# Kernel tuning notes

Measured on AMD Instinct MI355X. Metric: run time of the kernel, lower is better.

## Reference

```python
import jax, jax.numpy as jnp
import numpy as np

D_MODEL, N_HEADS, D_FF = 1024, 16, 4096
B, S = 2, 2048
EPS = 1e-6


def setup_inputs() -> dict:
    key = jax.random.key(0)
    ks = jax.random.split(key, 8)
    sc = 0.02
    x = jax.random.normal(ks[0], (B, S, D_MODEL), dtype=jnp.float32)
    Wq = jax.random.normal(ks[1], (D_MODEL, D_MODEL), dtype=jnp.float32) * sc
    Wk = jax.random.normal(ks[2], (D_MODEL, D_MODEL), dtype=jnp.float32) * sc
    Wv = jax.random.normal(ks[3], (D_MODEL, D_MODEL), dtype=jnp.float32) * sc
    Wo = jax.random.normal(ks[4], (D_MODEL, D_MODEL), dtype=jnp.float32) * sc
    W1 = jax.random.normal(ks[5], (D_MODEL, D_FF), dtype=jnp.float32) * sc
    W2 = jax.random.normal(ks[6], (D_FF, D_MODEL), dtype=jnp.float32) * sc
    z = lambda n: jnp.zeros((n,), dtype=jnp.float32)
    return {
        'x': x,
        'Wq': Wq, 'bq': z(D_MODEL), 'Wk': Wk, 'bk': z(D_MODEL),
        'Wv': Wv, 'bv': z(D_MODEL), 'Wo': Wo, 'bo': z(D_MODEL),
        'W1': W1, 'b1': z(D_FF), 'W2': W2, 'b2': z(D_MODEL),
        'alpha1': jnp.ones((D_MODEL,), jnp.float32), 'beta1': z(D_MODEL),
        'alpha2': jnp.ones((D_MODEL,), jnp.float32), 'beta2': z(D_MODEL),
    }


def _layernorm(y, alpha, beta):
    # torch.std is Bessel-corrected (N-1); original divides by (std + eps)
    d = y.shape[-1]
    m = jnp.mean(y, axis=-1, keepdims=True)
    c = y - m
    std = jnp.sqrt(jnp.sum(c * c, axis=-1, keepdims=True) / (d - 1))
    return alpha * c / (std + EPS) + beta


def reference(x, Wq, bq, Wk, bk, Wv, bv, Wo, bo, W1, b1, W2, b2,
              alpha1, beta1, alpha2, beta2):
    Bx, Sx, D = x.shape
    H = N_HEADS
    dk = D // H
    # projections -> [B, H, S, dk]
    q = (x @ Wq + bq).reshape(Bx, Sx, H, dk).transpose(0, 2, 1, 3)
    k = (x @ Wk + bk).reshape(Bx, Sx, H, dk).transpose(0, 2, 1, 3)
    v = (x @ Wv + bv).reshape(Bx, Sx, H, dk).transpose(0, 2, 1, 3)
    scores = jnp.einsum('bhqd,bhkd->bhqk', q, k) / np.sqrt(dk).astype(np.float32)
    attn = jax.nn.softmax(scores, axis=-1)  # [B, H, S, S]
    ctx = jnp.einsum('bhqk,bhkd->bhqd', attn, v)
    ctx = ctx.transpose(0, 2, 1, 3).reshape(Bx, Sx, D)
    attn_out = _layernorm(x + (ctx @ Wo + bo), alpha1, beta1)
    ff = jax.nn.relu(attn_out @ W1 + b1) @ W2 + b2
    enc_out = _layernorm(attn_out + ff, alpha2, beta2)
    return enc_out, attn
```

## Files before the change

kernel.cpp:

```cpp
#include <hip/hip_runtime.h>

typedef _Float16 h8 __attribute__((ext_vector_type(8)));
typedef float f4 __attribute__((ext_vector_type(4)));
typedef unsigned short u16;
typedef unsigned short us8 __attribute__((ext_vector_type(8)));

#define MFMA16(a, b, c) __builtin_amdgcn_mfma_f32_16x16x32_f16(a, b, c, 0, 0, 0)

static __device__ __forceinline__ float bf2f(u16 u) {
  unsigned int x = ((unsigned int)u) << 16;
  return __builtin_bit_cast(float, x);
}
static __device__ __forceinline__ u16 f2bf(float f) {
  unsigned int x = __builtin_bit_cast(unsigned int, f);
  x += 0x7fffu + ((x >> 16) & 1u);
  return (u16)(x >> 16);
}

static __device__ __forceinline__ void gload16(const void* g, void* l) {
  __builtin_amdgcn_global_load_lds((const __attribute__((address_space(1))) void*)g,
                                   (__attribute__((address_space(3))) void*)l, 16, 0, 0);
}

__global__ void detect_dtype(const void* __restrict__ alpha1, int* __restrict__ flag) {
  u16 u = ((const u16*)alpha1)[0];
  *flag = (u == 0x3F80u) ? 1 : (u == 0x3C00u ? 2 : 0);
}

__global__ __launch_bounds__(256) void cvt_to_f16(const void* __restrict__ in,
                                                  _Float16* __restrict__ out, int n,
                                                  const int* __restrict__ flag) {
  int f = *flag;
  int i = (blockIdx.x * 256 + threadIdx.x) * 8;
  if (i >= n) return;
  h8 o;
  if (f == 1) {
    us8 v = *(const us8*)((const u16*)in + i);
#pragma unroll
    for (int j = 0; j < 8; ++j) o[j] = (_Float16)bf2f(v[j]);
  } else if (f == 0) {
    const float* p = (const float*)in + i;
    f4 a = *(const f4*)p;
    f4 b = *(const f4*)(p + 4);
#pragma unroll
    for (int j = 0; j < 4; ++j) {
      o[j] = (_Float16)a[j];
      o[4 + j] = (_Float16)b[j];
    }
  } else {
    o = *(const h8*)((const _Float16*)in + i);
  }
  *(h8*)(out + i) = o;
}

__global__ __launch_bounds__(256) void cvt_vecs(const void* v0, const void* v1, const void* v2,
                                                const void* v3, const void* v4, const void* v5,
                                                const void* v6, const void* v7, const void* v8,
                                                const void* v9, float* __restrict__ out,
                                                const int* __restrict__ flag) {
  int i = blockIdx.x * 256 + threadIdx.x;
  if (i >= 13312) return;
  const void* src;
  int off;
  if (i < 4096) {
    src = (i < 1024) ? v0 : (i < 2048) ? v1 : (i < 3072) ? v2 : v3;
    off = i & 1023;
  } else if (i < 8192) {
    src = v4;
    off = i - 4096;
  } else {
    int j = (i - 8192) >> 10;
    src = (j == 0) ? v5 : (j == 1) ? v6 : (j == 2) ? v7 : (j == 3) ? v8 : v9;
    off = i & 1023;
  }
  int f = *flag;
  float val = (f == 1)   ? bf2f(((const u16*)src)[off])
              : (f == 0) ? ((const float*)src)[off]
                         : (float)((const _Float16*)src)[off];
  out[i] = val;
}

__global__ __launch_bounds__(256) void transpose_any(const void* __restrict__ W,
                                                     _Float16* __restrict__ Wt, int K, int N,
                                                     const int* __restrict__ flag) {
  int f = *flag;
  __shared__ _Float16 t[32][33];
  int n0 = blockIdx.x * 32, k0 = blockIdx.y * 32;
  int tx = threadIdx.x, ty = threadIdx.y;
#pragma unroll
  for (int i = 0; i < 4; ++i) {
    size_t idx = (size_t)(k0 + ty + 8 * i) * N + n0 + tx;
    float v = (f == 1)   ? bf2f(((const u16*)W)[idx])
              : (f == 0) ? ((const float*)W)[idx]
                         : (float)((const _Float16*)W)[idx];
    t[ty + 8 * i][tx] = (_Float16)v;
  }
  __syncthreads();
#pragma unroll
  for (int i = 0; i < 4; ++i)
    Wt[(size_t)(n0 + ty + 8 * i) * K + k0 + tx] = t[tx][ty + 8 * i];
}

__global__ __launch_bounds__(256) void transpose_v(const _Float16* __restrict__ V,
                                                   _Float16* __restrict__ Vt) {
  __shared__ _Float16 t[32][33];
  int s0 = blockIdx.x * 32, d0 = blockIdx.y * 32, bh = blockIdx.z;
  int b = bh >> 4, h = bh & 15;
  int tx = threadIdx.x, ty = threadIdx.y;
  const _Float16* src = V + (size_t)b * 2048 * 1024 + h * 64;
#pragma unroll
  for (int i = 0; i < 4; ++i)
    t[ty + 8 * i][tx] = src[(size_t)(s0 + ty + 8 * i) * 1024 + d0 + tx];
  __syncthreads();
  _Float16* dst = Vt + (size_t)bh * 64 * 2048;
#pragma unroll
  for (int i = 0; i < 4; ++i)
    dst[(size_t)(d0 + ty + 8 * i) * 2048 + s0 + tx] = t[tx][ty + 8 * i];
}

#define F_RELU 1
#define F_RES 2

__global__ __launch_bounds__(256, 2) void gemm_bt(const _Float16* __restrict__ A,
                                                  const _Float16* __restrict__ Bt,
                                                  const float* __restrict__ bias,
                                                  const _Float16* __restrict__ resid,
                                                  _Float16* __restrict__ C, int M, int N, int K,
                                                  int flags) {
  __shared__ __align__(16) _Float16 As[128][32];
  __shared__ __align__(16) _Float16 Bs[128][32];
  const int tid = threadIdx.x;
  const int lane = tid & 63, wave = tid >> 6;
  const int quad = lane >> 4, l15 = lane & 15;
  const int m0 = blockIdx.y * 128, n0 = blockIdx.x * 128;
  const int wm = (wave >> 1) * 64, wn = (wave & 1) * 64;

  f4 acc[4][4] = {};

  for (int k0 = 0; k0 < K; k0 += 32) {
    __syncthreads();
#pragma unroll
    for (int c = 0; c < 2; ++c) {
      int id = c * 256 + tid;
      int r = id >> 2, cc = id & 3;
      gload16(A + (size_t)(m0 + r) * K + k0 + cc * 8,
              (char*)&As[0][0] + c * 4096 + wave * 1024);
      gload16(Bt + (size_t)(n0 + r) * K + k0 + cc * 8,
              (char*)&Bs[0][0] + c * 4096 + wave * 1024);
    }
    __syncthreads();
    h8 a[4], b[4];
#pragma unroll
    for (int i = 0; i < 4; ++i) a[i] = *(const h8*)&As[wm + i * 16 + l15][quad * 8];
#pragma unroll
    for (int j = 0; j < 4; ++j) b[j] = *(const h8*)&Bs[wn + j * 16 + l15][quad * 8];
#pragma unroll
    for (int i = 0; i < 4; ++i)
#pragma unroll
      for (int j = 0; j < 4; ++j) acc[i][j] = MFMA16(a[i], b[j], acc[i][j]);
  }

#pragma unroll
  for (int j = 0; j < 4; ++j) {
    int col = n0 + wn + j * 16 + l15;
    float bi = bias[col];
#pragma unroll
    for (int i = 0; i < 4; ++i) {
      int rowb = m0 + wm + i * 16 + quad * 4;
#pragma unroll
      for (int r = 0; r < 4; ++r) {
        size_t off = (size_t)(rowb + r) * N + col;
        float v = acc[i][j][r] + bi;
        if (flags & F_RES) v += (float)resid[off];
        if (flags & F_RELU) v = fmaxf(v, 0.f);
        C[off] = (_Float16)v;
      }
    }
  }
}

__global__ __launch_bounds__(256, 2) void attn_kernel(const _Float16* __restrict__ Qm,
                                                      const _Float16* __restrict__ Km,
                                                      const _Float16* __restrict__ Vt,
                                                      void* __restrict__ d_out_all,
                                                      _Float16* __restrict__ ctx,
                                                      const int* __restrict__ flag) {
  const int S = 2048, D = 1024;
  const int q0 = blockIdx.x * 16;
  const int h = blockIdx.y, b = blockIdx.z;
  const int tid = threadIdx.x, lane = tid & 63, wave = tid >> 6;
  const int quad = lane >> 4, l15 = lane & 15;
  const float scale = 0.125f;
  const int f = *flag;

  const size_t base = (size_t)b * S * D + h * 64;
  const size_t vtbase = (size_t)(b * 16 + h) * 64 * S;
  const size_t eoff = 4194304ull + ((size_t)(b * 16 + h) * S + q0) * S;
  float* of = (float*)d_out_all + eoff;
  u16* ob = (u16*)d_out_all + eoff;
  _Float16* oh = (_Float16*)d_out_all + eoff;

  h8 aq0 = *(const h8*)(Qm + base + (size_t)(q0 + l15) * D + quad * 8);
  h8 aq1 = *(const h8*)(Qm + base + (size_t)(q0 + l15) * D + 32 + quad * 8);

  __shared__ float sl[4][16];
  __shared__ __align__(16) _Float16 Ps[4][16][40];
  __shared__ float red[4][16][64];

  float l_acc[4] = {0.f, 0.f, 0.f, 0.f};
  for (int it = 0; it < 32; ++it) {
    int n0 = (it * 4 + wave) * 16;
    h8 bk0 = *(const h8*)(Km + base + (size_t)(n0 + l15) * D + quad * 8);
    h8 bk1 = *(const h8*)(Km + base + (size_t)(n0 + l15) * D + 32 + quad * 8);
    f4 acc = {};
    acc = MFMA16(aq0, bk0, acc);
    acc = MFMA16(aq1, bk1, acc);
#pragma unroll
    for (int r = 0; r < 4; ++r) l_acc[r] += __expf(acc[r] * scale);
  }
#pragma unroll
  for (int r = 0; r < 4; ++r) {
#pragma unroll
    for (int msk = 1; msk < 16; msk <<= 1) l_acc[r] += __shfl_xor(l_acc[r], msk);
  }
  if (l15 == 0) {
#pragma unroll
    for (int r = 0; r < 4; ++r) sl[wave][quad * 4 + r] = l_acc[r];
  }
  __syncthreads();
  float li[4];
#pragma unroll
  for (int r = 0; r < 4; ++r) {
    int row = quad * 4 + r;
    li[r] = 1.f / (sl[0][row] + sl[1][row] + sl[2][row] + sl[3][row]);
  }

  f4 accv[4] = {};
  for (int it = 0; it < 16; ++it) {
    int k0 = (it * 4 + wave) * 32;
#pragma unroll
    for (int hh = 0; hh < 2; ++hh) {
      int n0 = k0 + hh * 16;
      h8 bk0 = *(const h8*)(Km + base + (size_t)(n0 + l15) * D + quad * 8);
      h8 bk1 = *(const h8*)(Km + base + (size_t)(n0 + l15) * D + 32 + quad * 8);
      f4 acc = {};
      acc = MFMA16(aq0, bk0, acc);
      acc = MFMA16(aq1, bk1, acc);
#pragma unroll
      for (int r = 0; r < 4; ++r) {
        float p = __expf(acc[r] * scale) * li[r];
        size_t aoff = (size_t)(quad * 4 + r) * S + n0 + l15;
        if (f == 0)
          __builtin_nontemporal_store(p, &of[aoff]);
        else if (f == 1)
          __builtin_nontemporal_store(f2bf(p), &ob[aoff]);
        else
          __builtin_nontemporal_store((_Float16)p, &oh[aoff]);
        Ps[wave][quad * 4 + r][hh * 16 + l15] = (_Float16)p;
      }
    }
    h8 ap = *(const h8*)&Ps[wave][l15][quad * 8];
#pragma unroll
    for (int nt = 0; nt < 4; ++nt) {
      h8 bv = *(const h8*)(Vt + vtbase + (size_t)(nt * 16 + l15) * S + k0 + quad * 8);
      accv[nt] = MFMA16(ap, bv, accv[nt]);
    }
  }
#pragma unroll
  for (int nt = 0; nt < 4; ++nt)
#pragma unroll
    for (int r = 0; r < 4; ++r) red[wave][quad * 4 + r][nt * 16 + l15] = accv[nt][r];
  __syncthreads();
  for (int x = tid; x < 1024; x += 256) {
    int row = x >> 6, col = x & 63;
    float v = red[0][row][col] + red[1][row][col] + red[2][row][col] + red[3][row][col];
    ctx[base + (size_t)(q0 + row) * D + col] = (_Float16)v;
  }
}

__global__ __launch_bounds__(256) void layernorm_k(const _Float16* __restrict__ Y,
                                                   const float* __restrict__ alpha,
                                                   const float* __restrict__ beta,
                                                   _Float16* __restrict__ outh,
                                                   void* __restrict__ outv,
                                                   const int* __restrict__ flag) {
  const int D = 1024;
  int row = blockIdx.x, tid = threadIdx.x;
  int wave = tid >> 6, lane = tid & 63;
  const _Float16* y = Y + (size_t)row * D;
  float v[4], s = 0.f;
#pragma unroll
  for (int j = 0; j < 4; ++j) {
    v[j] = (float)y[tid + 256 * j];
    s += v[j];
  }
#pragma unroll
  for (int msk = 1; msk < 64; msk <<= 1) s += __shfl_xor(s, msk);
  __shared__ float rs[4];
  if (lane == 0) rs[wave] = s;
  __syncthreads();
  s = rs[0] + rs[1] + rs[2] + rs[3];
  float mean = s * (1.f / 1024.f);
  float ss = 0.f;
#pragma unroll
  for (int j = 0; j < 4; ++j) {
    v[j] -= mean;
    ss += v[j] * v[j];
  }
#pragma unroll
  for (int msk = 1; msk < 64; msk <<= 1) ss += __shfl_xor(ss, msk);
  __syncthreads();
  if (lane == 0) rs[wave] = ss;
  __syncthreads();
  ss = rs[0] + rs[1] + rs[2] + rs[3];
  float inv = 1.f / (sqrtf(ss * (1.f / 1023.f)) + 1e-6f);
  int f = flag ? *flag : 0;
#pragma unroll
  for (int j = 0; j < 4; ++j) {
    int col = tid + 256 * j;
    float o = alpha[col] * v[j] * inv + beta[col];
    size_t off = (size_t)row * D + col;
    if (outh) outh[off] = (_Float16)o;
    if (outv) {
      if (f == 0)
        ((float*)outv)[off] = o;
      else if (f == 1)
        ((u16*)outv)[off] = f2bf(o);
      else
        ((_Float16*)outv)[off] = (_Float16)o;
    }
  }
}

#define WS_ELEMS (61ull * 1048576ull)
__device__ __attribute__((aligned(256))) _Float16 g_fb[WS_ELEMS];

extern "C" void kernel_launch(void* const* d_in, const int* in_sizes, int n_in, void* d_out,
                              int out_size, void* d_ws, size_t ws_size, hipStream_t stream) {
  const void* x = d_in[0];
  const void* Wq = d_in[1];
  const void* bq = d_in[2];
  const void* Wk = d_in[3];
  const void* bk = d_in[4];
  const void* Wv = d_in[5];
  const void* bv = d_in[6];
  const void* Wo = d_in[7];
  const void* bo = d_in[8];
  const void* W1 = d_in[9];
  const void* b1 = d_in[10];
  const void* W2 = d_in[11];
  const void* b2 = d_in[12];
  const void* alpha1 = d_in[13];
  const void* beta1 = d_in[14];
  const void* alpha2 = d_in[15];
  const void* beta2 = d_in[16];

  _Float16* ws;
  if (ws_size >= WS_ELEMS * sizeof(_Float16)) {
    ws = (_Float16*)d_ws;
  } else {
    void* p = nullptr;
    hipGetSymbolAddress(&p, HIP_SYMBOL(g_fb));
    ws = (_Float16*)p;
  }
  const size_t MEG = 1048576;
  _Float16* xh = ws;
  _Float16* WqT = ws + 4 * MEG;
  _Float16* WkT = ws + 5 * MEG;
  _Float16* WvT = ws + 6 * MEG;
  _Float16* WoT = ws + 7 * MEG;
  _Float16* W1T = ws + 8 * MEG;
  _Float16* W2T = ws + 12 * MEG;
  _Float16* qh = ws + 16 * MEG;
  _Float16* kh = ws + 20 * MEG;
  _Float16* vh = ws + 24 * MEG;
  _Float16* ctxh = ws + 28 * MEG;
  _Float16* y1h = ws + 32 * MEG;
  _Float16* aoh = ws + 36 * MEG;
  _Float16* hh = ws + 40 * MEG;
  _Float16* vth = ws + 40 * MEG;
  _Float16* y2h = ws + 56 * MEG;
  float* vecf = (float*)(ws + 60 * MEG);
  int* flag = (int*)(ws + 60 * MEG + 32768);

  const int BQ = 0, BK = 1024, BV = 2048, BO = 3072, B1 = 4096, B2 = 8192;
  const int A1 = 9216, BE1 = 10240, A2 = 11264, BE2 = 12288;

  detect_dtype<<<1, 1, 0, stream>>>(alpha1, flag);
  cvt_vecs<<<52, 256, 0, stream>>>(bq, bk, bv, bo, b1, b2, alpha1, beta1, alpha2, beta2, vecf,
                                   flag);
  cvt_to_f16<<<2048, 256, 0, stream>>>(x, xh, 4194304, flag);

  transpose_any<<<dim3(32, 32), dim3(32, 8), 0, stream>>>(Wq, WqT, 1024, 1024, flag);
  transpose_any<<<dim3(32, 32), dim3(32, 8), 0, stream>>>(Wk, WkT, 1024, 1024, flag);
  transpose_any<<<dim3(32, 32), dim3(32, 8), 0, stream>>>(Wv, WvT, 1024, 1024, flag);
  transpose_any<<<dim3(32, 32), dim3(32, 8), 0, stream>>>(Wo, WoT, 1024, 1024, flag);
  transpose_any<<<dim3(128, 32), dim3(32, 8), 0, stream>>>(W1, W1T, 1024, 4096, flag);
  transpose_any<<<dim3(32, 128), dim3(32, 8), 0, stream>>>(W2, W2T, 4096, 1024, flag);

  gemm_bt<<<dim3(8, 32), 256, 0, stream>>>(xh, WqT, vecf + BQ, nullptr, qh, 4096, 1024, 1024, 0);
  gemm_bt<<<dim3(8, 32), 256, 0, stream>>>(xh, WkT, vecf + BK, nullptr, kh, 4096, 1024, 1024, 0);
  gemm_bt<<<dim3(8, 32), 256, 0, stream>>>(xh, WvT, vecf + BV, nullptr, vh, 4096, 1024, 1024, 0);

  transpose_v<<<dim3(64, 2, 32), dim3(32, 8), 0, stream>>>(vh, vth);

  attn_kernel<<<dim3(128, 16, 2), 256, 0, stream>>>(qh, kh, vth, d_out, ctxh, flag);

  gemm_bt<<<dim3(8, 32), 256, 0, stream>>>(ctxh, WoT, vecf + BO, xh, y1h, 4096, 1024, 1024,
                                           F_RES);
  layernorm_k<<<4096, 256, 0, stream>>>(y1h, vecf + A1, vecf + BE1, aoh, nullptr, flag);

  gemm_bt<<<dim3(32, 32), 256, 0, stream>>>(aoh, W1T, vecf + B1, nullptr, hh, 4096, 4096, 1024,
                                            F_RELU);
  gemm_bt<<<dim3(8, 32), 256, 0, stream>>>(hh, W2T, vecf + B2, aoh, y2h, 4096, 1024, 4096,
                                           F_RES);
  layernorm_k<<<4096, 256, 0, stream>>>(y2h, vecf + A2, vecf + BE2, nullptr, d_out, flag);
}
```

Before: 1.159 ms.

## Fuse QKV GEMM, pack Q/K/V in MFMA fragment layout, cache exp scores

Merges the three Q/K/V projection GEMMs into a single GEMM with N=3072 and repacks Q, K and V into MFMA-fragment-contiguous layouts, so attention reads become fully coalesced 16-byte per-lane loads. The attention kernel now keeps the exponentiated scores from the first pass in registers as fp16, which removes the second QK^T recompute and K reload. The GEMM gains LDS double buffering so the next tile loads while the current one is in MFMAs. The costs are extra pack kernels, more registers (32 h4 values per lane) and fp16 rounding of the stored probabilities.

After: 983.9 us. 1.18x faster.

```diff
diff --git a/kernel.cpp b/kernel.cpp
--- a/kernel.cpp
+++ b/kernel.cpp
@@ -1,6 +1,7 @@
 #include <hip/hip_runtime.h>
 
 typedef _Float16 h8 __attribute__((ext_vector_type(8)));
+typedef _Float16 h4 __attribute__((ext_vector_type(4)));
 typedef float f4 __attribute__((ext_vector_type(4)));
 typedef unsigned short u16;
 typedef unsigned short us8 __attribute__((ext_vector_type(8)));
@@ -101,21 +102,36 @@
     Wt[(size_t)(n0 + ty + 8 * i) * K + k0 + tx] = t[tx][ty + 8 * i];
 }
 
-__global__ __launch_bounds__(256) void transpose_v(const _Float16* __restrict__ V,
-                                                   _Float16* __restrict__ Vt) {
-  __shared__ _Float16 t[32][33];
-  int s0 = blockIdx.x * 32, d0 = blockIdx.y * 32, bh = blockIdx.z;
+__global__ __launch_bounds__(256) void pack_qk(const _Float16* __restrict__ src,
+                                               _Float16* __restrict__ dst, int coloff) {
+  int id = blockIdx.x * 256 + threadIdx.x;
+  int lane = id & 63, rest = id >> 6;
+  int dt = rest & 1, st = (rest >> 1) & 127, bh = rest >> 8;
   int b = bh >> 4, h = bh & 15;
-  int tx = threadIdx.x, ty = threadIdx.y;
-  const _Float16* src = V + (size_t)b * 2048 * 1024 + h * 64;
-#pragma unroll
-  for (int i = 0; i < 4; ++i)
-    t[ty + 8 * i][tx] = src[(size_t)(s0 + ty + 8 * i) * 1024 + d0 + tx];
-  __syncthreads();
-  _Float16* dst = Vt + (size_t)bh * 64 * 2048;
-#pragma unroll
-  for (int i = 0; i < 4; ++i)
-    dst[(size_t)(d0 + ty + 8 * i) * 2048 + s0 + tx] = t[tx][ty + 8 * i];
+  int l15 = lane & 15, quad = lane >> 4;
+  h8 v = *(const h8*)(src + (size_t)(b * 2048 + st * 16 + l15) * 3072 + coloff + h * 64 +
+                      dt * 32 + quad * 8);
+  *(h8*)(dst + (size_t)id * 8) = v;
+}
+
+__global__ __launch_bounds__(256) void pack_v(const _Float16* __restrict__ src,
+                                              _Float16* __restrict__ dst) {
+  __shared__ _Float16 t[32][72];
+  int kt = blockIdx.x, bh = blockIdx.y;
+  int b = bh >> 4, h = bh & 15;
+  int tid = threadIdx.x;
+  {
+    int sl = tid >> 3, dp = (tid & 7) * 8;
+    h8 v = *(const h8*)(src + (size_t)(b * 2048 + kt * 32 + sl) * 3072 + 2048 + h * 64 + dp);
+    *(h8*)&t[sl][dp] = v;
+  }
+  __syncthreads();
+  int nt = tid >> 6, lane = tid & 63;
+  int l15 = lane & 15, quad = lane >> 4;
+  h8 o;
+#pragma unroll
+  for (int j = 0; j < 8; ++j) o[j] = t[quad * 8 + j][nt * 16 + l15];
+  *(h8*)(dst + (size_t)bh * 131072 + kt * 2048 + (size_t)tid * 8) = o;
 }
 
 #define F_RELU 1
@@ -127,8 +143,8 @@
                                                   const _Float16* __restrict__ resid,
                                                   _Float16* __restrict__ C, int M, int N, int K,
                                                   int flags) {
-  __shared__ __align__(16) _Float16 As[128][32];
-  __shared__ __align__(16) _Float16 Bs[128][32];
+  __shared__ __align__(16) _Float16 As[2][128][32];
+  __shared__ __align__(16) _Float16 Bs[2][128][32];
   const int tid = threadIdx.x;
   const int lane = tid & 63, wave = tid >> 6;
   const int quad = lane >> 4, l15 = lane & 15;
@@ -137,28 +153,36 @@
 
   f4 acc[4][4] = {};
 
+#define STAGE(buf, kk)                                                              \
+  do {                                                                              \
+    _Pragma("unroll") for (int c = 0; c < 2; ++c) {                                 \
+      int id = c * 256 + tid;                                                       \
+      int r = id >> 2, cc = id & 3;                                                 \
+      gload16(A + (size_t)(m0 + r) * K + (kk) + cc * 8,                             \
+              (char*)&As[buf][0][0] + c * 4096 + wave * 1024);                      \
+      gload16(Bt + (size_t)(n0 + r) * K + (kk) + cc * 8,                            \
+              (char*)&Bs[buf][0][0] + c * 4096 + wave * 1024);                      \
+    }                                                                               \
+  } while (0)
+
+  STAGE(0, 0);
+  __syncthreads();
+  int cur = 0;
   for (int k0 = 0; k0 < K; k0 += 32) {
+    if (k0 + 32 < K) STAGE(cur ^ 1, k0 + 32);
+    h8 a[4], b[4];
+#pragma unroll
+    for (int i = 0; i < 4; ++i) a[i] = *(const h8*)&As[cur][wm + i * 16 + l15][quad * 8];
+#pragma unroll
+    for (int j = 0; j < 4; ++j) b[j] = *(const h8*)&Bs[cur][wn + j * 16 + l15][quad * 8];
+#pragma unroll
+    for (int i = 0; i < 4; ++i)
+#pragma unroll
+      for (int j = 0; j < 4; ++j) acc[i][j] = MFMA16(a[i], b[j], acc[i][j]);
     __syncthreads();
-#pragma unroll
-    for (int c = 0; c < 2; ++c) {
-      int id = c * 256 + tid;
-      int r = id >> 2, cc = id & 3;
-      gload16(A + (size_t)(m0 + r) * K + k0 + cc * 8,
-              (char*)&As[0][0] + c * 4096 + wave * 1024);
-      gload16(Bt + (size_t)(n0 + r) * K + k0 + cc * 8,
-              (char*)&Bs[0][0] + c * 4096 + wave * 1024);
-    }
-    __syncthreads();
-    h8 a[4], b[4];
-#pragma unroll
-    for (int i = 0; i < 4; ++i) a[i] = *(const h8*)&As[wm + i * 16 + l15][quad * 8];
-#pragma unroll
-    for (int j = 0; j < 4; ++j) b[j] = *(const h8*)&Bs[wn + j * 16 + l15][quad * 8];
-#pragma unroll
-    for (int i = 0; i < 4; ++i)
-#pragma unroll
-      for (int j = 0; j < 4; ++j) acc[i][j] = MFMA16(a[i], b[j], acc[i][j]);
-  }
+    cur ^= 1;
+  }
+#undef STAGE
 
 #pragma unroll
   for (int j = 0; j < 4; ++j) {
@@ -179,44 +203,52 @@
   }
 }
 
-__global__ __launch_bounds__(256, 2) void attn_kernel(const _Float16* __restrict__ Qm,
-                                                      const _Float16* __restrict__ Km,
-                                                      const _Float16* __restrict__ Vt,
+__global__ __launch_bounds__(256, 2) void attn_kernel(const _Float16* __restrict__ Qf,
+                                                      const _Float16* __restrict__ Kf,
+                                                      const _Float16* __restrict__ Vf,
                                                       void* __restrict__ d_out_all,
                                                       _Float16* __restrict__ ctx,
                                                       const int* __restrict__ flag) {
   const int S = 2048, D = 1024;
   const int q0 = blockIdx.x * 16;
   const int h = blockIdx.y, b = blockIdx.z;
+  const int bh = b * 16 + h;
   const int tid = threadIdx.x, lane = tid & 63, wave = tid >> 6;
   const int quad = lane >> 4, l15 = lane & 15;
   const float scale = 0.125f;
   const int f = *flag;
 
-  const size_t base = (size_t)b * S * D + h * 64;
-  const size_t vtbase = (size_t)(b * 16 + h) * 64 * S;
-  const size_t eoff = 4194304ull + ((size_t)(b * 16 + h) * S + q0) * S;
+  const size_t fbase = (size_t)bh * 131072;
+  const size_t eoff = 4194304ull + ((size_t)bh * S + q0) * S;
   float* of = (float*)d_out_all + eoff;
   u16* ob = (u16*)d_out_all + eoff;
   _Float16* oh = (_Float16*)d_out_all + eoff;
 
-  h8 aq0 = *(const h8*)(Qm + base + (size_t)(q0 + l15) * D + quad * 8);
-  h8 aq1 = *(const h8*)(Qm + base + (size_t)(q0 + l15) * D + 32 + quad * 8);
+  h8 aq0 = *(const h8*)(Qf + fbase + (size_t)(q0 >> 4) * 1024 + lane * 8);
+  h8 aq1 = *(const h8*)(Qf + fbase + (size_t)(q0 >> 4) * 1024 + 512 + lane * 8);
 
   __shared__ float sl[4][16];
   __shared__ __align__(16) _Float16 Ps[4][16][40];
   __shared__ float red[4][16][64];
 
+  h4 pc[32];
   float l_acc[4] = {0.f, 0.f, 0.f, 0.f};
+#pragma unroll
   for (int it = 0; it < 32; ++it) {
-    int n0 = (it * 4 + wave) * 16;
-    h8 bk0 = *(const h8*)(Km + base + (size_t)(n0 + l15) * D + quad * 8);
-    h8 bk1 = *(const h8*)(Km + base + (size_t)(n0 + l15) * D + 32 + quad * 8);
+    int st = wave * 32 + it;
+    h8 bk0 = *(const h8*)(Kf + fbase + (size_t)st * 1024 + lane * 8);
+    h8 bk1 = *(const h8*)(Kf + fbase + (size_t)st * 1024 + 512 + lane * 8);
     f4 acc = {};
     acc = MFMA16(aq0, bk0, acc);
     acc = MFMA16(aq1, bk1, acc);
-#pragma unroll
-    for (int r = 0; r < 4; ++r) l_acc[r] += __expf(acc[r] * scale);
+    h4 t;
+#pragma unroll
+    for (int r = 0; r < 4; ++r) {
+      float e = __expf(acc[r] * scale);
+      l_acc[r] += e;
+      t[r] = (_Float16)e;
+    }
+    pc[it] = t;
   }
 #pragma unroll
   for (int r = 0; r < 4; ++r) {
@@ -236,20 +268,16 @@
   }
 
   f4 accv[4] = {};
-  for (int it = 0; it < 16; ++it) {
-    int k0 = (it * 4 + wave) * 32;
+#pragma unroll
+  for (int it2 = 0; it2 < 16; ++it2) {
+    int k0 = wave * 512 + it2 * 32;
 #pragma unroll
     for (int hh = 0; hh < 2; ++hh) {
-      int n0 = k0 + hh * 16;
-      h8 bk0 = *(const h8*)(Km + base + (size_t)(n0 + l15) * D + quad * 8);
-      h8 bk1 = *(const h8*)(Km + base + (size_t)(n0 + l15) * D + 32 + quad * 8);
-      f4 acc = {};
-      acc = MFMA16(aq0, bk0, acc);
-      acc = MFMA16(aq1, bk1, acc);
+      h4 t = pc[it2 * 2 + hh];
 #pragma unroll
       for (int r = 0; r < 4; ++r) {
-        float p = __expf(acc[r] * scale) * li[r];
-        size_t aoff = (size_t)(quad * 4 + r) * S + n0 + l15;
+        float p = (float)t[r] * li[r];
+        size_t aoff = (size_t)(quad * 4 + r) * S + k0 + hh * 16 + l15;
         if (f == 0)
           __builtin_nontemporal_store(p, &of[aoff]);
         else if (f == 1)
@@ -260,9 +288,10 @@
       }
     }
     h8 ap = *(const h8*)&Ps[wave][l15][quad * 8];
+    int kt = k0 >> 5;
 #pragma unroll
     for (int nt = 0; nt < 4; ++nt) {
-      h8 bv = *(const h8*)(Vt + vtbase + (size_t)(nt * 16 + l15) * S + k0 + quad * 8);
+      h8 bv = *(const h8*)(Vf + fbase + (size_t)kt * 2048 + nt * 512 + lane * 8);
       accv[nt] = MFMA16(ap, bv, accv[nt]);
     }
   }
@@ -271,10 +300,11 @@
 #pragma unroll
     for (int r = 0; r < 4; ++r) red[wave][quad * 4 + r][nt * 16 + l15] = accv[nt][r];
   __syncthreads();
+  const size_t cbase = (size_t)b * S * D + h * 64;
   for (int x = tid; x < 1024; x += 256) {
     int row = x >> 6, col = x & 63;
     float v = red[0][row][col] + red[1][row][col] + red[2][row][col] + red[3][row][col];
-    ctx[base + (size_t)(q0 + row) * D + col] = (_Float16)v;
+    ctx[cbase + (size_t)(q0 + row) * D + col] = (_Float16)v;
   }
 }
 
@@ -365,25 +395,23 @@
   }
   const size_t MEG = 1048576;
   _Float16* xh = ws;
-  _Float16* WqT = ws + 4 * MEG;
-  _Float16* WkT = ws + 5 * MEG;
-  _Float16* WvT = ws + 6 * MEG;
+  _Float16* WqkvT = ws + 4 * MEG;
   _Float16* WoT = ws + 7 * MEG;
   _Float16* W1T = ws + 8 * MEG;
   _Float16* W2T = ws + 12 * MEG;
-  _Float16* qh = ws + 16 * MEG;
-  _Float16* kh = ws + 20 * MEG;
-  _Float16* vh = ws + 24 * MEG;
-  _Float16* ctxh = ws + 28 * MEG;
-  _Float16* y1h = ws + 32 * MEG;
-  _Float16* aoh = ws + 36 * MEG;
-  _Float16* hh = ws + 40 * MEG;
-  _Float16* vth = ws + 40 * MEG;
-  _Float16* y2h = ws + 56 * MEG;
+  _Float16* qkvh = ws + 16 * MEG;
+  _Float16* Qf = ws + 28 * MEG;
+  _Float16* Kf = ws + 32 * MEG;
+  _Float16* Vf = ws + 36 * MEG;
+  _Float16* ctxh = ws + 40 * MEG;
+  _Float16* y1h = ws + 44 * MEG;
+  _Float16* aoh = ws + 48 * MEG;
+  _Float16* hh = ws + 16 * MEG;
+  _Float16* y2h = ws + 52 * MEG;
   float* vecf = (float*)(ws + 60 * MEG);
   int* flag = (int*)(ws + 60 * MEG + 32768);
 
-  const int BQ = 0, BK = 1024, BV = 2048, BO = 3072, B1 = 4096, B2 = 8192;
+  const int BQ = 0, BO = 3072, B1 = 4096, B2 = 8192;
   const int A1 = 9216, BE1 = 10240, A2 = 11264, BE2 = 12288;
 
   detect_dtype<<<1, 1, 0, stream>>>(alpha1, flag);
@@ -391,20 +419,23 @@
                                    flag);
   cvt_to_f16<<<2048, 256, 0, stream>>>(x, xh, 4194304, flag);
 
-  transpose_any<<<dim3(32, 32), dim3(32, 8), 0, stream>>>(Wq, WqT, 1024, 1024, flag);
-  transpose_any<<<dim3(32, 32), dim3(32, 8), 0, stream>>>(Wk, WkT, 1024, 1024, flag);
-  transpose_any<<<dim3(32, 32), dim3(32, 8), 0, stream>>>(Wv, WvT, 1024, 1024, flag);
+  transpose_any<<<dim3(32, 32), dim3(32, 8), 0, stream>>>(Wq, WqkvT, 1024, 1024, flag);
+  transpose_any<<<dim3(32, 32), dim3(32, 8), 0, stream>>>(Wk, WqkvT + 1024 * 1024, 1024, 1024,
+                                                          flag);
+  transpose_any<<<dim3(32, 32), dim3(32, 8), 0, stream>>>(Wv, WqkvT + 2 * 1024 * 1024, 1024,
+                                                          1024, flag);
   transpose_any<<<dim3(32, 32), dim3(32, 8), 0, stream>>>(Wo, WoT, 1024, 1024, flag);
   transpose_any<<<dim3(128, 32), dim3(32, 8), 0, stream>>>(W1, W1T, 1024, 4096, flag);
   transpose_any<<<dim3(32, 128), dim3(32, 8), 0, stream>>>(W2, W2T, 4096, 1024, flag);
 
-  gemm_bt<<<dim3(8, 32), 256, 0, stream>>>(xh, WqT, vecf + BQ, nullptr, qh, 4096, 1024, 1024, 0);
-  gemm_bt<<<dim3(8, 32), 256, 0, stream>>>(xh, WkT, vecf + BK, nullptr, kh, 4096, 1024, 1024, 0);
-  gemm_bt<<<dim3(8, 32), 256, 0, stream>>>(xh, WvT, vecf + BV, nullptr, vh, 4096, 1024, 1024, 0);
-
-  transpose_v<<<dim3(64, 2, 32), dim3(32, 8), 0, stream>>>(vh, vth);
-
-  attn_kernel<<<dim3(128, 16, 2), 256, 0, stream>>>(qh, kh, vth, d_out, ctxh, flag);
+  gemm_bt<<<dim3(24, 32), 256, 0, stream>>>(xh, WqkvT, vecf + BQ, nullptr, qkvh, 4096, 3072,
+                                            1024, 0);
+
+  pack_qk<<<4096, 256, 0, stream>>>(qkvh, Qf, 0);
+  pack_qk<<<4096, 256, 0, stream>>>(qkvh, Kf, 1024);
+  pack_v<<<dim3(64, 32), 256, 0, stream>>>(qkvh, Vf);
+
+  attn_kernel<<<dim3(128, 16, 2), 256, 0, stream>>>(Qf, Kf, Vf, d_out, ctxh, flag);
 
   gemm_bt<<<dim3(8, 32), 256, 0, stream>>>(ctxh, WoT, vecf + BO, xh, y1h, 4096, 1024, 1024,
                                            F_RES);
```
